# Kernel tuning notes

Measured on AMD Instinct MI355X. Metric: run time of the kernel, lower is better.

The kernel has to match this reference:

```python
import jax, jax.numpy as jnp
import numpy as np
from jax import lax

H = W = 128          # feature map size (gen_line_map uses 128x128)
C = 128              # dim_loi
NPTS0 = 32           # n_pts0 samples per line
NPTS1 = 8            # after MaxPool1d(4, stride=4)
TOPK = 50            # n_dyn_junc
SCALE = 5.0          # proposal_lines distance scale


def proposal_lines(md_maps, dis_maps, scale=SCALE):
    h, w = md_maps.shape[1], md_maps.shape[2]
    y0, x0 = jnp.meshgrid(jnp.arange(h, dtype=jnp.float32),
                          jnp.arange(w, dtype=jnp.float32), indexing='ij')
    md_ = (md_maps[0] - 0.5) * np.pi * 2
    st_ = md_maps[1] * np.pi / 2
    ed_ = -md_maps[2] * np.pi / 2
    cs_md, ss_md = jnp.cos(md_), jnp.sin(md_)
    cs_st = jnp.clip(jnp.cos(st_), 0.001, None)
    ss_st = jnp.clip(jnp.sin(st_), 0.001, None)
    cs_ed = jnp.clip(jnp.cos(ed_), 0.001, None)
    ss_ed = jnp.clip(jnp.sin(ed_), None, -0.001)
    y_st = ss_st / cs_st
    y_ed = ss_ed / cs_ed
    d = dis_maps[0] * scale
    x_st = (cs_md - ss_md * y_st) * d
    y_s = (ss_md + cs_md * y_st) * d
    x_ed = (cs_md - ss_md * y_ed) * d
    y_e = (ss_md + cs_md * y_ed) * d
    x_st_f = jnp.clip(x_st + x0, 0.0, w - 1)
    y_st_f = jnp.clip(y_s + y0, 0.0, h - 1)
    x_ed_f = jnp.clip(x_ed + x0, 0.0, w - 1)
    y_ed_f = jnp.clip(y_e + y0, 0.0, h - 1)
    return jnp.stack((x_st_f, y_st_f, x_ed_f, y_ed_f), axis=-1).reshape(-1, 4)


def pooling(feats, lines):
    # feats: [C, H, W]; lines: [N, 4]
    h, w = feats.shape[1], feats.shape[2]
    tspan = jnp.linspace(0.0, 1.0, NPTS0)[None, None, :]           # [1,1,32]
    U, V = lines[:, :2], lines[:, 2:]
    sp = U[:, :, None] * tspan + V[:, :, None] * (1 - tspan) - 0.5  # [N,2,32]
    sp = sp.transpose(0, 2, 1).reshape(-1, 2)                       # [N*32, 2]
    px, py = sp[:, 0], sp[:, 1]
    px0 = jnp.clip(jnp.floor(px), 0.0, w - 1)
    py0 = jnp.clip(jnp.floor(py), 0.0, h - 1)
    px1 = jnp.clip(px0 + 1, 0.0, w - 1)
    py1 = jnp.clip(py0 + 1, 0.0, h - 1)
    px0l, py0l = px0.astype(jnp.int32), py0.astype(jnp.int32)
    px1l, py1l = px1.astype(jnp.int32), py1.astype(jnp.int32)
    # bilinear gather-weight, fused in a single expression: [C, N*32]
    xp = (feats[:, py0l, px0l] * (py1 - py) * (px1 - px)
          + feats[:, py1l, px0l] * (py - py0) * (px1 - px)
          + feats[:, py0l, px1l] * (py1 - py) * (px - px0)
          + feats[:, py1l, px1l] * (py - py0) * (px - px0))
    xp = xp.reshape(C, -1, NPTS0).transpose(1, 0, 2)                # [N, C, 32]
    xp = xp.reshape(xp.shape[0], C, NPTS1, NPTS0 // NPTS1).max(-1)  # MaxPool1d(4,4)
    return xp.reshape(-1, NPTS1 * C)                                # [N, 1024]


def nms(a):
    # F.max_pool2d(a, 3, stride=1, padding=1) then keep local maxima
    ap = lax.reduce_window(a, -jnp.inf, lax.max, (1, 3, 3), (1, 1, 1), 'SAME')
    return a * (a == ap).astype(a.dtype)


def get_junctions(jloc_nms, joff, topk=TOPK):
    h, w = jloc_nms.shape[1], jloc_nms.shape[2]
    scores, index = lax.top_k(jloc_nms.reshape(-1), topk)
    jf = joff.reshape(2, -1)
    y = (index // w).astype(jnp.float32) + jf[1][index] + 0.5
    x = (index % w).astype(jnp.float32) + jf[0][index] + 0.5
    juncs = jnp.stack((x, y), axis=1)                               # [topk, 2]
    return juncs, scores, index


def setup_inputs() -> dict:
    key = jax.random.key(0)
    ks = jax.random.split(key, 12)
    return {
        'md': jax.random.uniform(ks[0], (3, H, W), dtype=jnp.float32),
        'dis': jax.random.uniform(ks[1], (1, H, W), dtype=jnp.float32),
        'res': jax.random.uniform(ks[2], (1, H, W), dtype=jnp.float32),
        'jloc': jax.random.uniform(ks[3], (1, H, W), dtype=jnp.float32),
        'joff': jax.random.uniform(ks[4], (2, H, W), dtype=jnp.float32) - 0.5,
        'feats': jax.random.normal(ks[5], (C, H, W), dtype=jnp.float32),
        'W1': jax.random.normal(ks[6], (1024, C * NPTS1), dtype=jnp.float32) * 0.02,
        'b1': jax.random.normal(ks[7], (1024,), dtype=jnp.float32) * 0.02,
        'W2': jax.random.normal(ks[8], (1024, 1024), dtype=jnp.float32) * 0.02,
        'b2': jax.random.normal(ks[9], (1024,), dtype=jnp.float32) * 0.02,
        'W3': jax.random.normal(ks[10], (1, 1024), dtype=jnp.float32) * 0.02,
        'b3': jax.random.normal(ks[11], (1,), dtype=jnp.float32) * 0.02,
    }


def reference(md, dis, res, jloc, joff, feats, W1, b1, W2, b2, W3, b3):
    # line proposals at 3 residual scales (use_residual=True)
    lines = jnp.concatenate([
        proposal_lines(md, dis + s * res) for s in (-1.0, 0.0, 1.0)
    ], axis=0)                                                      # [3*H*W, 4]
    # LOI bilinear pooling + scoring MLP (self.fc)
    x = pooling(feats, lines)                                       # [N, 1024]
    x = jax.nn.relu(x @ W1.T + b1)
    x = jax.nn.relu(x @ W2.T + b2)
    logits = x @ W3.T + b3                                          # [N, 1]
    # junction decode: NMS + topk + offset gather
    juncs, jscores, _ = get_junctions(nms(jloc), joff, TOPK)
    return logits, juncs, jscores
```

## Files before the change

kernel.cpp:

```cpp
#include <hip/hip_runtime.h>
#include <hip/hip_bf16.h>
#include <math.h>

#define HH 128
#define WW 128
#define HW 16384
#define NL 49152
#define CC 128
#define NPTS0 32
#define NPTS1 8
#define PI_F 3.14159265358979323846f

typedef __attribute__((ext_vector_type(8))) short short8;
typedef __attribute__((ext_vector_type(4))) float f32x4;

__device__ __forceinline__ ushort f2bf(float f) {
    unsigned u = __builtin_bit_cast(unsigned, f);
    unsigned rounding = 0x7FFFu + ((u >> 16) & 1u);
    return (ushort)((u + rounding) >> 16);
}

__device__ __forceinline__ void gload_lds16(const void* gsrc, void* ldst) {
    __builtin_amdgcn_global_load_lds(
        (const __attribute__((address_space(1))) unsigned int*)gsrc,
        (__attribute__((address_space(3))) unsigned int*)ldst,
        16, 0, 0);
}

__device__ __forceinline__ void unpk8(uint4 d, float* f) {
    f[0] = __builtin_bit_cast(float, d.x << 16);
    f[1] = __builtin_bit_cast(float, d.x & 0xFFFF0000u);
    f[2] = __builtin_bit_cast(float, d.y << 16);
    f[3] = __builtin_bit_cast(float, d.y & 0xFFFF0000u);
    f[4] = __builtin_bit_cast(float, d.z << 16);
    f[5] = __builtin_bit_cast(float, d.z & 0xFFFF0000u);
    f[6] = __builtin_bit_cast(float, d.w << 16);
    f[7] = __builtin_bit_cast(float, d.w & 0xFFFF0000u);
}

__global__ __launch_bounds__(256) void k_lines(
    const float* __restrict__ md, const float* __restrict__ dis,
    const float* __restrict__ res, float* __restrict__ lines)
{
    int g = blockIdx.x * 256 + threadIdx.x;
    if (g >= NL) return;
    int s = g / HW;
    int pix = g - s * HW;
    float sf = (float)(s - 1);
    int y = pix >> 7, x = pix & 127;

    float md0 = md[pix], md1 = md[HW + pix], md2 = md[2 * HW + pix];
    float d = (dis[pix] + sf * res[pix]) * 5.0f;

    float md_ = (md0 - 0.5f) * (2.0f * PI_F);
    float st_ = md1 * (0.5f * PI_F);
    float ed_ = -md2 * (0.5f * PI_F);
    float cs_md = cosf(md_), ss_md = sinf(md_);
    float cs_st = fmaxf(cosf(st_), 0.001f);
    float ss_st = fmaxf(sinf(st_), 0.001f);
    float cs_ed = fmaxf(cosf(ed_), 0.001f);
    float ss_ed = fminf(sinf(ed_), -0.001f);
    float y_st = ss_st / cs_st;
    float y_ed = ss_ed / cs_ed;
    float x_st = (cs_md - ss_md * y_st) * d;
    float y_s  = (ss_md + cs_md * y_st) * d;
    float x_ed = (cs_md - ss_md * y_ed) * d;
    float y_e  = (ss_md + cs_md * y_ed) * d;

    float4 o;
    o.x = fminf(fmaxf(x_st + (float)x, 0.0f), 127.0f);
    o.y = fminf(fmaxf(y_s  + (float)y, 0.0f), 127.0f);
    o.z = fminf(fmaxf(x_ed + (float)x, 0.0f), 127.0f);
    o.w = fminf(fmaxf(y_e  + (float)y, 0.0f), 127.0f);
    ((float4*)lines)[g] = o;
}

__global__ void k_transpose(const float* __restrict__ in, ushort* __restrict__ out)
{
    __shared__ float tile[32][33];
    int cb = blockIdx.x;
    int pb = blockIdx.y;
    int tx = threadIdx.x, ty = threadIdx.y;
#pragma unroll
    for (int j = 0; j < 32; j += 8)
        tile[ty + j][tx] = in[(size_t)(cb * 32 + ty + j) * HW + pb * 32 + tx];
    __syncthreads();
#pragma unroll
    for (int j = 0; j < 32; j += 8)
        out[(size_t)(pb * 32 + ty + j) * CC + cb * 32 + tx] = f2bf(tile[tx][ty + j]);
}

__global__ void k_cvt(const float* __restrict__ a, const float* __restrict__ b,
                      ushort* __restrict__ oa, ushort* __restrict__ ob, int n)
{
    int i = blockIdx.x * 256 + threadIdx.x;
    if (i < n) { oa[i] = f2bf(a[i]); ob[i] = f2bf(b[i]); }
}

__global__ __launch_bounds__(128, 2) void k_pool(
    const ushort* __restrict__ ft, const float* __restrict__ lines,
    ushort* __restrict__ X)
{
    __shared__ __align__(16) unsigned smeta[2048];
    const int t = threadIdx.x;
    const int l_loc = t >> 4, c8 = t & 15;
    const int gl0 = blockIdx.x * 8;

#pragma unroll
    for (int e = 0; e < 2; ++e) {
        int s = t + e * 128;
        int ml = s >> 5, sp = s & 31;
        float4 L = ((const float4*)lines)[gl0 + ml];
        float tf = (float)sp * (1.0f / 31.0f);
        float omt = 1.0f - tf;
        float px = L.x * tf + L.z * omt - 0.5f;
        float py = L.y * tf + L.w * omt - 0.5f;
        float px0 = fminf(fmaxf(floorf(px), 0.0f), 127.0f);
        float py0 = fminf(fmaxf(floorf(py), 0.0f), 127.0f);
        float px1 = fminf(px0 + 1.0f, 127.0f);
        float py1 = fminf(py0 + 1.0f, 127.0f);
        int ix0 = (int)px0, iy0 = (int)py0, ix1 = (int)px1, iy1 = (int)py1;
        float4 wv;
        wv.x = (py1 - py) * (px1 - px);
        wv.y = (py  - py0) * (px1 - px);
        wv.z = (py1 - py) * (px  - px0);
        wv.w = (py  - py0) * (px  - px0);
        int o00 = (iy0 * WW + ix0) * (CC * 2);
        int dx  = (ix1 - ix0) * (CC * 2);
        int dy  = (iy1 - iy0) * (WW * CC * 2);
        int4 ov;
        ov.x = o00;
        ov.y = o00 + dy;
        ov.z = o00 + dx;
        ov.w = o00 + dy + dx;
        *(float4*)&smeta[s * 8]     = wv;
        *(int4*)  &smeta[s * 8 + 4] = ov;
    }
    __syncthreads();

    const unsigned coff = (unsigned)(c8 * 16);
    const char* fbase = (const char*)ft;
    float m[8][8];
#pragma unroll
    for (int ch = 0; ch < 8; ++ch)
#pragma unroll
        for (int g = 0; g < 8; ++g) m[ch][g] = -INFINITY;

#pragma unroll
    for (int g = 0; g < 8; ++g) {
#pragma unroll
        for (int j = 0; j < 4; ++j) {
            const unsigned* mp = &smeta[(l_loc * 32 + g * 4 + j) * 8];
            float4 wv = *(const float4*)mp;
            int4  ov = *(const int4*)(mp + 4);
            uint4 d00 = *(const uint4*)(fbase + ((unsigned)ov.x + coff));
            uint4 d10 = *(const uint4*)(fbase + ((unsigned)ov.y + coff));
            uint4 d01 = *(const uint4*)(fbase + ((unsigned)ov.z + coff));
            uint4 d11 = *(const uint4*)(fbase + ((unsigned)ov.w + coff));
            float f00[8], f10[8], f01[8], f11[8];
            unpk8(d00, f00); unpk8(d10, f10); unpk8(d01, f01); unpk8(d11, f11);
#pragma unroll
            for (int ch = 0; ch < 8; ++ch) {
                float v = f00[ch] * wv.x + f10[ch] * wv.y
                        + f01[ch] * wv.z + f11[ch] * wv.w;
                m[ch][g] = fmaxf(m[ch][g], v);
            }
        }
    }

    ushort* Xp = X + (size_t)(gl0 + l_loc) * 1024 + c8 * 64;
#pragma unroll
    for (int ch = 0; ch < 8; ++ch) {
        short8 pk;
#pragma unroll
        for (int g = 0; g < 8; ++g) pk[g] = (short)f2bf(m[ch][g]);
        *(short8*)(Xp + ch * 8) = pk;
    }
}

#define NIT 8
template<int EPI>
__global__ __launch_bounds__(512, 1) void k_gemm2(
    const ushort* __restrict__ A, const ushort* __restrict__ B,
    const float* __restrict__ bias, ushort* __restrict__ Y,
    const float* __restrict__ w3, float* __restrict__ logits,
    int M, int N, int K)
{
    __shared__ __align__(16) ushort lds[65536];
    const int tid = threadIdx.x;
    const int w = tid >> 6, l = tid & 63;
    const int lr = l & 15, kq = l >> 4;
    const int wm = w >> 2, wn = w & 3;

    const int nwg = gridDim.x;
    const int cpx = nwg >> 3;
    const int swzb = (blockIdx.x & 7) * cpx + (blockIdx.x >> 3);
    const int nbn = N >> 8;
    const int m_blk = swzb / nbn;
    const int n_blk = swzb % nbn;
    const int m0 = m_blk << 8, n0 = n_blk << 8;

    const ushort* pA = A + (size_t)m0 * K;
    const ushort* pB = B + (size_t)n0 * K;

    const int rS = tid >> 3;
    const int gS = (tid & 7) ^ (rS & 7);

#define STG(gp, rowoff, kt, regbase) { \
    gload_lds16((gp) + (size_t)((rowoff) + rS) * K + (kt) * 64 + gS * 8, \
                &lds[(regbase) + tid * 8]); \
    gload_lds16((gp) + (size_t)((rowoff) + 64 + rS) * K + (kt) * 64 + gS * 8, \
                &lds[(regbase) + 4096 + tid * 8]); }

#define FBAR { __builtin_amdgcn_sched_barrier(0); __builtin_amdgcn_s_barrier(); \
               __builtin_amdgcn_sched_barrier(0); }

    const int swz0 = ((kq) ^ (lr & 7)) * 8;
    const int swz1 = ((4 + kq) ^ (lr & 7)) * 8;
    int aoff[8], boff[4];
#pragma unroll
    for (int m = 0; m < 8; ++m) aoff[m] = (wm * 128 + m * 16 + lr) * 64;
#pragma unroll
    for (int n = 0; n < 4; ++n) boff[n] = 16384 + (wn * 64 + n * 16 + lr) * 64;

    f32x4 acc[8][4] = {};
    short8 bq0, bq1, bq2, bq3;

#define MF16(MLO, A0, A1, A2, A3) \
    acc[MLO+0][0] = __builtin_amdgcn_mfma_f32_16x16x32_bf16(bq0, A0, acc[MLO+0][0], 0, 0, 0); \
    acc[MLO+0][1] = __builtin_amdgcn_mfma_f32_16x16x32_bf16(bq1, A0, acc[MLO+0][1], 0, 0, 0); \
    acc[MLO+0][2] = __builtin_amdgcn_mfma_f32_16x16x32_bf16(bq2, A0, acc[MLO+0][2], 0, 0, 0); \
    acc[MLO+0][3] = __builtin_amdgcn_mfma_f32_16x16x32_bf16(bq3, A0, acc[MLO+0][3], 0, 0, 0); \
    acc[MLO+1][0] = __builtin_amdgcn_mfma_f32_16x16x32_bf16(bq0, A1, acc[MLO+1][0], 0, 0, 0); \
    acc[MLO+1][1] = __builtin_amdgcn_mfma_f32_16x16x32_bf16(bq1, A1, acc[MLO+1][1], 0, 0, 0); \
    acc[MLO+1][2] = __builtin_amdgcn_mfma_f32_16x16x32_bf16(bq2, A1, acc[MLO+1][2], 0, 0, 0); \
    acc[MLO+1][3] = __builtin_amdgcn_mfma_f32_16x16x32_bf16(bq3, A1, acc[MLO+1][3], 0, 0, 0); \
    acc[MLO+2][0] = __builtin_amdgcn_mfma_f32_16x16x32_bf16(bq0, A2, acc[MLO+2][0], 0, 0, 0); \
    acc[MLO+2][1] = __builtin_amdgcn_mfma_f32_16x16x32_bf16(bq1, A2, acc[MLO+2][1], 0, 0, 0); \
    acc[MLO+2][2] = __builtin_amdgcn_mfma_f32_16x16x32_bf16(bq2, A2, acc[MLO+2][2], 0, 0, 0); \
    acc[MLO+2][3] = __builtin_amdgcn_mfma_f32_16x16x32_bf16(bq3, A2, acc[MLO+2][3], 0, 0, 0); \
    acc[MLO+3][0] = __builtin_amdgcn_mfma_f32_16x16x32_bf16(bq0, A3, acc[MLO+3][0], 0, 0, 0); \
    acc[MLO+3][1] = __builtin_amdgcn_mfma_f32_16x16x32_bf16(bq1, A3, acc[MLO+3][1], 0, 0, 0); \
    acc[MLO+3][2] = __builtin_amdgcn_mfma_f32_16x16x32_bf16(bq2, A3, acc[MLO+3][2], 0, 0, 0); \
    acc[MLO+3][3] = __builtin_amdgcn_mfma_f32_16x16x32_bf16(bq3, A3, acc[MLO+3][3], 0, 0, 0);

    STG(pA, 0,   0, 0);
    STG(pA, 128, 0, 8192);
    STG(pB, 0,   0, 16384);
    STG(pB, 128, 0, 24576);
    STG(pB, 0,   1, 49152);
    asm volatile("s_waitcnt vmcnt(2)" ::: "memory");
    FBAR;

    for (int i = 0; i < NIT; ++i) {
        const int t1 = 2 * i + 1, t2 = 2 * i + 2, t3 = 2 * i + 3;
        const bool pf = (i < NIT - 1);

        bq0 = *(const short8*)&lds[boff[0] + swz0];
        bq1 = *(const short8*)&lds[boff[1] + swz0];
        bq2 = *(const short8*)&lds[boff[2] + swz0];
        bq3 = *(const short8*)&lds[boff[3] + swz0];
        {
            short8 a0 = *(const short8*)&lds[aoff[0] + swz0];
            short8 a1 = *(const short8*)&lds[aoff[1] + swz0];
            short8 a2 = *(const short8*)&lds[aoff[2] + swz0];
            short8 a3 = *(const short8*)&lds[aoff[3] + swz0];
            STG(pB, 128, t1, 57344);
            FBAR;
            __builtin_amdgcn_s_setprio(1); MF16(0, a0, a1, a2, a3) __builtin_amdgcn_s_setprio(0);
            FBAR;
        }
        {
            short8 a4 = *(const short8*)&lds[aoff[4] + swz0];
            short8 a5 = *(const short8*)&lds[aoff[5] + swz0];
            short8 a6 = *(const short8*)&lds[aoff[6] + swz0];
            short8 a7 = *(const short8*)&lds[aoff[7] + swz0];
            STG(pA, 0, t1, 32768);
            FBAR;
            __builtin_amdgcn_s_setprio(1); MF16(4, a4, a5, a6, a7) __builtin_amdgcn_s_setprio(0);
            FBAR;
        }
        bq0 = *(const short8*)&lds[boff[0] + swz1];
        bq1 = *(const short8*)&lds[boff[1] + swz1];
        bq2 = *(const short8*)&lds[boff[2] + swz1];
        bq3 = *(const short8*)&lds[boff[3] + swz1];
        {
            short8 a0 = *(const short8*)&lds[aoff[0] + swz1];
            short8 a1 = *(const short8*)&lds[aoff[1] + swz1];
            short8 a2 = *(const short8*)&lds[aoff[2] + swz1];
            short8 a3 = *(const short8*)&lds[aoff[3] + swz1];
            STG(pA, 128, t1, 40960);
            FBAR;
            __builtin_amdgcn_s_setprio(1); MF16(0, a0, a1, a2, a3) __builtin_amdgcn_s_setprio(0);
            FBAR;
        }
        {
            short8 a4 = *(const short8*)&lds[aoff[4] + swz1];
            short8 a5 = *(const short8*)&lds[aoff[5] + swz1];
            short8 a6 = *(const short8*)&lds[aoff[6] + swz1];
            short8 a7 = *(const short8*)&lds[aoff[7] + swz1];
            if (pf) STG(pB, 0, t2, 16384);
            FBAR;
            __builtin_amdgcn_s_setprio(1); MF16(4, a4, a5, a6, a7) __builtin_amdgcn_s_setprio(0);
            if (pf) { asm volatile("s_waitcnt vmcnt(2)" ::: "memory"); }
            else    { asm volatile("s_waitcnt vmcnt(0)" ::: "memory"); }
            FBAR;
        }
        bq0 = *(const short8*)&lds[32768 + boff[0] + swz0];
        bq1 = *(const short8*)&lds[32768 + boff[1] + swz0];
        bq2 = *(const short8*)&lds[32768 + boff[2] + swz0];
        bq3 = *(const short8*)&lds[32768 + boff[3] + swz0];
        {
            short8 a0 = *(const short8*)&lds[32768 + aoff[0] + swz0];
            short8 a1 = *(const short8*)&lds[32768 + aoff[1] + swz0];
            short8 a2 = *(const short8*)&lds[32768 + aoff[2] + swz0];
            short8 a3 = *(const short8*)&lds[32768 + aoff[3] + swz0];
            if (pf) STG(pB, 128, t2, 24576);
            FBAR;
            __builtin_amdgcn_s_setprio(1); MF16(0, a0, a1, a2, a3) __builtin_amdgcn_s_setprio(0);
            FBAR;
        }
        {
            short8 a4 = *(const short8*)&lds[32768 + aoff[4] + swz0];
            short8 a5 = *(const short8*)&lds[32768 + aoff[5] + swz0];
            short8 a6 = *(const short8*)&lds[32768 + aoff[6] + swz0];
            short8 a7 = *(const short8*)&lds[32768 + aoff[7] + swz0];
            if (pf) STG(pA, 0, t2, 0);
            FBAR;
            __builtin_amdgcn_s_setprio(1); MF16(4, a4, a5, a6, a7) __builtin_amdgcn_s_setprio(0);
            FBAR;
        }
        bq0 = *(const short8*)&lds[32768 + boff[0] + swz1];
        bq1 = *(const short8*)&lds[32768 + boff[1] + swz1];
        bq2 = *(const short8*)&lds[32768 + boff[2] + swz1];
        bq3 = *(const short8*)&lds[32768 + boff[3] + swz1];
        {
            short8 a0 = *(const short8*)&lds[32768 + aoff[0] + swz1];
            short8 a1 = *(const short8*)&lds[32768 + aoff[1] + swz1];
            short8 a2 = *(const short8*)&lds[32768 + aoff[2] + swz1];
            short8 a3 = *(const short8*)&lds[32768 + aoff[3] + swz1];
            if (pf) STG(pA, 128, t2, 8192);
            FBAR;
            __builtin_amdgcn_s_setprio(1); MF16(0, a0, a1, a2, a3) __builtin_amdgcn_s_setprio(0);
            FBAR;
        }
        {
            short8 a4 = *(const short8*)&lds[32768 + aoff[4] + swz1];
            short8 a5 = *(const short8*)&lds[32768 + aoff[5] + swz1];
            short8 a6 = *(const short8*)&lds[32768 + aoff[6] + swz1];
            short8 a7 = *(const short8*)&lds[32768 + aoff[7] + swz1];
            if (pf) STG(pB, 0, t3, 49152);
            FBAR;
            __builtin_amdgcn_s_setprio(1); MF16(4, a4, a5, a6, a7) __builtin_amdgcn_s_setprio(0);
            if (pf) { asm volatile("s_waitcnt vmcnt(2)" ::: "memory"); }
            FBAR;
        }
    }
#undef STG
#undef FBAR
#undef MF16

    if (EPI == 0) {
#pragma unroll
        for (int n = 0; n < 4; ++n) {
            int cbase = n0 + wn * 64 + n * 16 + kq * 4;
            float4 bv4 = *(const float4*)&bias[cbase];
#pragma unroll
            for (int m = 0; m < 8; ++m) {
                int row = m0 + wm * 128 + m * 16 + lr;
                ushort4 pk;
                pk.x = f2bf(fmaxf(acc[m][n][0] + bv4.x, 0.0f));
                pk.y = f2bf(fmaxf(acc[m][n][1] + bv4.y, 0.0f));
                pk.z = f2bf(fmaxf(acc[m][n][2] + bv4.z, 0.0f));
                pk.w = f2bf(fmaxf(acc[m][n][3] + bv4.w, 0.0f));
                *(ushort4*)(Y + (size_t)row * N + cbase) = pk;
            }
        }
    } else {
        float4 bv4[4], w34[4];
#pragma unroll
        for (int n = 0; n < 4; ++n) {
            int cbase = n0 + wn * 64 + n * 16 + kq * 4;
            bv4[n] = *(const float4*)&bias[cbase];
            w34[n] = *(const float4*)&w3[cbase];
        }
#pragma unroll
        for (int m = 0; m < 8; ++m) {
            float s = 0.0f;
#pragma unroll
            for (int n = 0; n < 4; ++n) {
                s += fmaxf(acc[m][n][0] + bv4[n].x, 0.0f) * w34[n].x;
                s += fmaxf(acc[m][n][1] + bv4[n].y, 0.0f) * w34[n].y;
                s += fmaxf(acc[m][n][2] + bv4[n].z, 0.0f) * w34[n].z;
                s += fmaxf(acc[m][n][3] + bv4[n].w, 0.0f) * w34[n].w;
            }
            s += __shfl_xor(s, 16, 64);
            s += __shfl_xor(s, 32, 64);
            if (kq == 0)
                atomicAdd(&logits[m0 + wm * 128 + m * 16 + lr], s);
        }
    }
}

__global__ void k_init_logits(float* __restrict__ logits, const float* __restrict__ b3, int n)
{
    int i = blockIdx.x * 256 + threadIdx.x;
    if (i < n) logits[i] = b3[0];
}

__global__ __launch_bounds__(256) void k_nms_topk(
    const float* __restrict__ jloc, unsigned long long* __restrict__ cand)
{
    __shared__ unsigned long long sk[256];
    const int t = threadIdx.x;
    const int idx = blockIdx.x * 256 + t;
    const int y = idx >> 7, x = idx & 127;
    float cv = jloc[idx];
    float m = cv;
    for (int dy = -1; dy <= 1; ++dy) {
        int yy = y + dy;
        if (yy < 0 || yy > 127) continue;
        for (int dx = -1; dx <= 1; ++dx) {
            int xx = x + dx;
            if (xx < 0 || xx > 127) continue;
            m = fmaxf(m, jloc[(yy << 7) + xx]);
        }
    }
    float nv = (cv == m) ? cv : 0.0f;
    unsigned vb = __builtin_bit_cast(unsigned, nv);
    sk[t] = ((unsigned long long)vb << 32) | (unsigned)(0xFFFFFFFFu - idx);
    __syncthreads();
    for (int k = 2; k <= 256; k <<= 1) {
        for (int j = k >> 1; j >= 1; j >>= 1) {
            int ixj = t ^ j;
            if (ixj > t) {
                unsigned long long a = sk[t], b = sk[ixj];
                bool up = ((t & k) == 0);
                if (up ? (a < b) : (a > b)) { sk[t] = b; sk[ixj] = a; }
            }
            __syncthreads();
        }
    }
    if (t < 64) cand[blockIdx.x * 64 + t] = (t < 50) ? sk[t] : 0ull;
}

__global__ __launch_bounds__(1024) void k_topk_final(
    const unsigned long long* __restrict__ cand,
    const float* __restrict__ joff, float* __restrict__ outj)
{
    __shared__ unsigned long long sk[4096];
    const int t = threadIdx.x;
#pragma unroll
    for (int e = 0; e < 4; ++e) sk[t + (e << 10)] = cand[t + (e << 10)];
    __syncthreads();
    for (int k = 2; k <= 4096; k <<= 1) {
        for (int j = k >> 1; j >= 1; j >>= 1) {
#pragma unroll
            for (int e = 0; e < 4; ++e) {
                int i = t + (e << 10);
                int ixj = i ^ j;
                if (ixj > i) {
                    unsigned long long a = sk[i], b = sk[ixj];
                    bool up = ((i & k) == 0);
                    if (up ? (a < b) : (a > b)) { sk[i] = b; sk[ixj] = a; }
                }
            }
            __syncthreads();
        }
    }
    if (t < 50) {
        unsigned long long kk = sk[t];
        unsigned idx = 0xFFFFFFFFu - (unsigned)(kk & 0xFFFFFFFFull);
        float val = __builtin_bit_cast(float, (unsigned)(kk >> 32));
        int y = idx >> 7, x = idx & 127;
        outj[2 * t]     = (float)x + joff[idx]      + 0.5f;
        outj[2 * t + 1] = (float)y + joff[HW + idx] + 0.5f;
        outj[100 + t]   = val;
    }
}

extern "C" void kernel_launch(void* const* d_in, const int* in_sizes, int n_in,
                              void* d_out, int out_size, void* d_ws, size_t ws_size,
                              hipStream_t stream) {
    const float* md   = (const float*)d_in[0];
    const float* dis  = (const float*)d_in[1];
    const float* res  = (const float*)d_in[2];
    const float* jloc = (const float*)d_in[3];
    const float* joff = (const float*)d_in[4];
    const float* feats= (const float*)d_in[5];
    const float* W1   = (const float*)d_in[6];
    const float* b1   = (const float*)d_in[7];
    const float* W2   = (const float*)d_in[8];
    const float* b2   = (const float*)d_in[9];
    const float* W3   = (const float*)d_in[10];
    const float* b3   = (const float*)d_in[11];
    float* out = (float*)d_out;

    char* ws = (char*)d_ws;
    size_t off = 0;
    auto alloc = [&](size_t bytes) {
        void* p = ws + off;
        off = (off + bytes + 255) & ~(size_t)255;
        return p;
    };
    float*  lines = (float*) alloc((size_t)NL * 4 * sizeof(float));
    ushort* ft    = (ushort*)alloc((size_t)HW * CC * 2);
    ushort* W1b   = (ushort*)alloc((size_t)1024 * 1024 * 2);
    ushort* W2b   = (ushort*)alloc((size_t)1024 * 1024 * 2);
    ushort* X     = (ushort*)alloc((size_t)NL * 1024 * 2);
    ushort* Y1    = (ushort*)alloc((size_t)NL * 1024 * 2);
    unsigned long long* cand = (unsigned long long*)alloc(4096 * 8);

    k_lines<<<NL / 256, 256, 0, stream>>>(md, dis, res, lines);
    k_transpose<<<dim3(CC / 32, HW / 32), dim3(32, 8), 0, stream>>>(feats, ft);
    k_cvt<<<(1024 * 1024) / 256, 256, 0, stream>>>(W1, W2, W1b, W2b, 1024 * 1024);
    k_pool<<<NL / 8, 128, 0, stream>>>(ft, lines, X);

    int ngrid = (NL / 256) * (1024 / 256);
    k_gemm2<0><<<ngrid, 512, 0, stream>>>(X, W1b, b1, Y1, nullptr, nullptr, NL, 1024, 1024);
    k_init_logits<<<NL / 256, 256, 0, stream>>>(out, b3, NL);
    k_gemm2<1><<<ngrid, 512, 0, stream>>>(Y1, W2b, b2, nullptr, W3, out, NL, 1024, 1024);

    k_nms_topk<<<64, 256, 0, stream>>>(jloc, cand);
    k_topk_final<<<1, 1024, 0, stream>>>(cand, joff, out + NL);
}
```

Measured before the change: 350.4 us.

## Split GEMM 256x256 tile across 16 waves instead of 8

Runs each 256x256 GEMM tile with 1024 threads (16 waves) rather than 512, so each wave owns a 64x64 sub-tile with half the accumulators. Each thread now issues one global-to-LDS load per stage instead of two, and the vmcnt waits are adjusted to match. The aim is more waves per CU to hide LDS and memory latency. The cost is more barrier participants, more LDS reads per MFMA since each wave reuses its B fragments over fewer A rows, and a register budget capped by the 1024-thread launch bound.

```diff
diff --git a/kernel.cpp b/kernel.cpp
--- a/kernel.cpp
+++ b/kernel.cpp
@@ -180,7 +180,7 @@
 
 #define NIT 8
 template<int EPI>
-__global__ __launch_bounds__(512, 1) void k_gemm2(
+__global__ __launch_bounds__(1024) void k_gemm2(
     const ushort* __restrict__ A, const ushort* __restrict__ B,
     const float* __restrict__ bias, ushort* __restrict__ Y,
     const float* __restrict__ w3, float* __restrict__ logits,
@@ -206,27 +206,25 @@
     const int rS = tid >> 3;
     const int gS = (tid & 7) ^ (rS & 7);
 
-#define STG(gp, rowoff, kt, regbase) { \
+#define STG(gp, rowoff, kt, regbase) \
     gload_lds16((gp) + (size_t)((rowoff) + rS) * K + (kt) * 64 + gS * 8, \
-                &lds[(regbase) + tid * 8]); \
-    gload_lds16((gp) + (size_t)((rowoff) + 64 + rS) * K + (kt) * 64 + gS * 8, \
-                &lds[(regbase) + 4096 + tid * 8]); }
+                &lds[(regbase) + tid * 8]);
 
 #define FBAR { __builtin_amdgcn_sched_barrier(0); __builtin_amdgcn_s_barrier(); \
                __builtin_amdgcn_sched_barrier(0); }
 
     const int swz0 = ((kq) ^ (lr & 7)) * 8;
     const int swz1 = ((4 + kq) ^ (lr & 7)) * 8;
-    int aoff[8], boff[4];
-#pragma unroll
-    for (int m = 0; m < 8; ++m) aoff[m] = (wm * 128 + m * 16 + lr) * 64;
+    int aoff[4], boff[4];
+#pragma unroll
+    for (int m = 0; m < 4; ++m) aoff[m] = (wm * 64 + m * 16 + lr) * 64;
 #pragma unroll
     for (int n = 0; n < 4; ++n) boff[n] = 16384 + (wn * 64 + n * 16 + lr) * 64;
 
-    f32x4 acc[8][4] = {};
+    f32x4 acc[4][4] = {};
     short8 bq0, bq1, bq2, bq3;
 
-#define MF16(MLO, A0, A1, A2, A3) \
+#define MF8(MLO, A0, A1) \
     acc[MLO+0][0] = __builtin_amdgcn_mfma_f32_16x16x32_bf16(bq0, A0, acc[MLO+0][0], 0, 0, 0); \
     acc[MLO+0][1] = __builtin_amdgcn_mfma_f32_16x16x32_bf16(bq1, A0, acc[MLO+0][1], 0, 0, 0); \
     acc[MLO+0][2] = __builtin_amdgcn_mfma_f32_16x16x32_bf16(bq2, A0, acc[MLO+0][2], 0, 0, 0); \
@@ -234,22 +232,14 @@
     acc[MLO+1][0] = __builtin_amdgcn_mfma_f32_16x16x32_bf16(bq0, A1, acc[MLO+1][0], 0, 0, 0); \
     acc[MLO+1][1] = __builtin_amdgcn_mfma_f32_16x16x32_bf16(bq1, A1, acc[MLO+1][1], 0, 0, 0); \
     acc[MLO+1][2] = __builtin_amdgcn_mfma_f32_16x16x32_bf16(bq2, A1, acc[MLO+1][2], 0, 0, 0); \
-    acc[MLO+1][3] = __builtin_amdgcn_mfma_f32_16x16x32_bf16(bq3, A1, acc[MLO+1][3], 0, 0, 0); \
-    acc[MLO+2][0] = __builtin_amdgcn_mfma_f32_16x16x32_bf16(bq0, A2, acc[MLO+2][0], 0, 0, 0); \
-    acc[MLO+2][1] = __builtin_amdgcn_mfma_f32_16x16x32_bf16(bq1, A2, acc[MLO+2][1], 0, 0, 0); \
-    acc[MLO+2][2] = __builtin_amdgcn_mfma_f32_16x16x32_bf16(bq2, A2, acc[MLO+2][2], 0, 0, 0); \
-    acc[MLO+2][3] = __builtin_amdgcn_mfma_f32_16x16x32_bf16(bq3, A2, acc[MLO+2][3], 0, 0, 0); \
-    acc[MLO+3][0] = __builtin_amdgcn_mfma_f32_16x16x32_bf16(bq0, A3, acc[MLO+3][0], 0, 0, 0); \
-    acc[MLO+3][1] = __builtin_amdgcn_mfma_f32_16x16x32_bf16(bq1, A3, acc[MLO+3][1], 0, 0, 0); \
-    acc[MLO+3][2] = __builtin_amdgcn_mfma_f32_16x16x32_bf16(bq2, A3, acc[MLO+3][2], 0, 0, 0); \
-    acc[MLO+3][3] = __builtin_amdgcn_mfma_f32_16x16x32_bf16(bq3, A3, acc[MLO+3][3], 0, 0, 0);
+    acc[MLO+1][3] = __builtin_amdgcn_mfma_f32_16x16x32_bf16(bq3, A1, acc[MLO+1][3], 0, 0, 0);
 
     STG(pA, 0,   0, 0);
     STG(pA, 128, 0, 8192);
     STG(pB, 0,   0, 16384);
     STG(pB, 128, 0, 24576);
     STG(pB, 0,   1, 49152);
-    asm volatile("s_waitcnt vmcnt(2)" ::: "memory");
+    asm volatile("s_waitcnt vmcnt(1)" ::: "memory");
     FBAR;
 
     for (int i = 0; i < NIT; ++i) {
@@ -263,21 +253,17 @@
         {
             short8 a0 = *(const short8*)&lds[aoff[0] + swz0];
             short8 a1 = *(const short8*)&lds[aoff[1] + swz0];
+            STG(pB, 128, t1, 57344);
+            FBAR;
+            __builtin_amdgcn_s_setprio(1); MF8(0, a0, a1) __builtin_amdgcn_s_setprio(0);
+            FBAR;
+        }
+        {
             short8 a2 = *(const short8*)&lds[aoff[2] + swz0];
             short8 a3 = *(const short8*)&lds[aoff[3] + swz0];
-            STG(pB, 128, t1, 57344);
-            FBAR;
-            __builtin_amdgcn_s_setprio(1); MF16(0, a0, a1, a2, a3) __builtin_amdgcn_s_setprio(0);
-            FBAR;
-        }
-        {
-            short8 a4 = *(const short8*)&lds[aoff[4] + swz0];
-            short8 a5 = *(const short8*)&lds[aoff[5] + swz0];
-            short8 a6 = *(const short8*)&lds[aoff[6] + swz0];
-            short8 a7 = *(const short8*)&lds[aoff[7] + swz0];
             STG(pA, 0, t1, 32768);
             FBAR;
-            __builtin_amdgcn_s_setprio(1); MF16(4, a4, a5, a6, a7) __builtin_amdgcn_s_setprio(0);
+            __builtin_amdgcn_s_setprio(1); MF8(2, a2, a3) __builtin_amdgcn_s_setprio(0);
             FBAR;
         }
         bq0 = *(const short8*)&lds[boff[0] + swz1];
@@ -287,22 +273,18 @@
         {
             short8 a0 = *(const short8*)&lds[aoff[0] + swz1];
             short8 a1 = *(const short8*)&lds[aoff[1] + swz1];
+            STG(pA, 128, t1, 40960);
+            FBAR;
+            __builtin_amdgcn_s_setprio(1); MF8(0, a0, a1) __builtin_amdgcn_s_setprio(0);
+            FBAR;
+        }
+        {
             short8 a2 = *(const short8*)&lds[aoff[2] + swz1];
             short8 a3 = *(const short8*)&lds[aoff[3] + swz1];
-            STG(pA, 128, t1, 40960);
-            FBAR;
-            __builtin_amdgcn_s_setprio(1); MF16(0, a0, a1, a2, a3) __builtin_amdgcn_s_setprio(0);
-            FBAR;
-        }
-        {
-            short8 a4 = *(const short8*)&lds[aoff[4] + swz1];
-            short8 a5 = *(const short8*)&lds[aoff[5] + swz1];
-            short8 a6 = *(const short8*)&lds[aoff[6] + swz1];
-            short8 a7 = *(const short8*)&lds[aoff[7] + swz1];
             if (pf) STG(pB, 0, t2, 16384);
             FBAR;
-            __builtin_amdgcn_s_setprio(1); MF16(4, a4, a5, a6, a7) __builtin_amdgcn_s_setprio(0);
-            if (pf) { asm volatile("s_waitcnt vmcnt(2)" ::: "memory"); }
+            __builtin_amdgcn_s_setprio(1); MF8(2, a2, a3) __builtin_amdgcn_s_setprio(0);
+            if (pf) { asm volatile("s_waitcnt vmcnt(1)" ::: "memory"); }
             else    { asm volatile("s_waitcnt vmcnt(0)" ::: "memory"); }
             FBAR;
         }
@@ -313,21 +295,17 @@
         {
             short8 a0 = *(const short8*)&lds[32768 + aoff[0] + swz0];
             short8 a1 = *(const short8*)&lds[32768 + aoff[1] + swz0];
+            if (pf) STG(pB, 128, t2, 24576);
+            FBAR;
+            __builtin_amdgcn_s_setprio(1); MF8(0, a0, a1) __builtin_amdgcn_s_setprio(0);
+            FBAR;
+        }
+        {
             short8 a2 = *(const short8*)&lds[32768 + aoff[2] + swz0];
             short8 a3 = *(const short8*)&lds[32768 + aoff[3] + swz0];
-            if (pf) STG(pB, 128, t2, 24576);
-            FBAR;
-            __builtin_amdgcn_s_setprio(1); MF16(0, a0, a1, a2, a3) __builtin_amdgcn_s_setprio(0);
-            FBAR;
-        }
-        {
-            short8 a4 = *(const short8*)&lds[32768 + aoff[4] + swz0];
-            short8 a5 = *(const short8*)&lds[32768 + aoff[5] + swz0];
-            short8 a6 = *(const short8*)&lds[32768 + aoff[6] + swz0];
-            short8 a7 = *(const short8*)&lds[32768 + aoff[7] + swz0];
             if (pf) STG(pA, 0, t2, 0);
             FBAR;
-            __builtin_amdgcn_s_setprio(1); MF16(4, a4, a5, a6, a7) __builtin_amdgcn_s_setprio(0);
+            __builtin_amdgcn_s_setprio(1); MF8(2, a2, a3) __builtin_amdgcn_s_setprio(0);
             FBAR;
         }
         bq0 = *(const short8*)&lds[32768 + boff[0] + swz1];
@@ -337,28 +315,24 @@
         {
             short8 a0 = *(const short8*)&lds[32768 + aoff[0] + swz1];
             short8 a1 = *(const short8*)&lds[32768 + aoff[1] + swz1];
+            if (pf) STG(pA, 128, t2, 8192);
+            FBAR;
+            __builtin_amdgcn_s_setprio(1); MF8(0, a0, a1) __builtin_amdgcn_s_setprio(0);
+            FBAR;
+        }
+        {
             short8 a2 = *(const short8*)&lds[32768 + aoff[2] + swz1];
             short8 a3 = *(const short8*)&lds[32768 + aoff[3] + swz1];
-            if (pf) STG(pA, 128, t2, 8192);
-            FBAR;
-            __builtin_amdgcn_s_setprio(1); MF16(0, a0, a1, a2, a3) __builtin_amdgcn_s_setprio(0);
-            FBAR;
-        }
-        {
-            short8 a4 = *(const short8*)&lds[32768 + aoff[4] + swz1];
-            short8 a5 = *(const short8*)&lds[32768 + aoff[5] + swz1];
-            short8 a6 = *(const short8*)&lds[32768 + aoff[6] + swz1];
-            short8 a7 = *(const short8*)&lds[32768 + aoff[7] + swz1];
             if (pf) STG(pB, 0, t3, 49152);
             FBAR;
-            __builtin_amdgcn_s_setprio(1); MF16(4, a4, a5, a6, a7) __builtin_amdgcn_s_setprio(0);
-            if (pf) { asm volatile("s_waitcnt vmcnt(2)" ::: "memory"); }
+            __builtin_amdgcn_s_setprio(1); MF8(2, a2, a3) __builtin_amdgcn_s_setprio(0);
+            if (pf) { asm volatile("s_waitcnt vmcnt(1)" ::: "memory"); }
             FBAR;
         }
     }
 #undef STG
 #undef FBAR
-#undef MF16
+#undef MF8
 
     if (EPI == 0) {
 #pragma unroll
@@ -366,8 +340,8 @@
             int cbase = n0 + wn * 64 + n * 16 + kq * 4;
             float4 bv4 = *(const float4*)&bias[cbase];
 #pragma unroll
-            for (int m = 0; m < 8; ++m) {
-                int row = m0 + wm * 128 + m * 16 + lr;
+            for (int m = 0; m < 4; ++m) {
+                int row = m0 + wm * 64 + m * 16 + lr;
                 ushort4 pk;
                 pk.x = f2bf(fmaxf(acc[m][n][0] + bv4.x, 0.0f));
                 pk.y = f2bf(fmaxf(acc[m][n][1] + bv4.y, 0.0f));
@@ -385,7 +359,7 @@
             w34[n] = *(const float4*)&w3[cbase];
         }
 #pragma unroll
-        for (int m = 0; m < 8; ++m) {
+        for (int m = 0; m < 4; ++m) {
             float s = 0.0f;
 #pragma unroll
             for (int n = 0; n < 4; ++n) {
@@ -397,7 +371,7 @@
             s += __shfl_xor(s, 16, 64);
             s += __shfl_xor(s, 32, 64);
             if (kq == 0)
-                atomicAdd(&logits[m0 + wm * 128 + m * 16 + lr], s);
+                atomicAdd(&logits[m0 + wm * 64 + m * 16 + lr], s);
         }
     }
 }
@@ -517,9 +491,9 @@
     k_pool<<<NL / 8, 128, 0, stream>>>(ft, lines, X);
 
     int ngrid = (NL / 256) * (1024 / 256);
-    k_gemm2<0><<<ngrid, 512, 0, stream>>>(X, W1b, b1, Y1, nullptr, nullptr, NL, 1024, 1024);
+    k_gemm2<0><<<ngrid, 1024, 0, stream>>>(X, W1b, b1, Y1, nullptr, nullptr, NL, 1024, 1024);
     k_init_logits<<<NL / 256, 256, 0, stream>>>(out, b3, NL);
-    k_gemm2<1><<<ngrid, 512, 0, stream>>>(Y1, W2b, b2, nullptr, W3, out, NL, 1024, 1024);
+    k_gemm2<1><<<ngrid, 1024, 0, stream>>>(Y1, W2b, b2, nullptr, W3, out, NL, 1024, 1024);
 
     k_nms_topk<<<64, 256, 0, stream>>>(jloc, cand);
     k_topk_final<<<1, 1024, 0, stream>>>(cand, joff, out + NL);
```

New measurement: 384.4 us. +9.7%, slower.

## Make GEMM persistent over three M tiles with continuous cross-tile prefetch

Applied to the files above, without the earlier changes.

Grid goes from 768 to 256 workgroups (one per CU on MI355X). Each workgroup walks three consecutive 256-row M tiles against a fixed 256-column N tile, running 24 K-iterations instead of 8. The global-to-LDS prefetch pipeline runs across tile boundaries. The epilogue (bias, ReLU, store or logit dot-product) and accumulator reset are done in-loop every 8 iterations. This is meant to remove the tail effect of 3 waves and the pipeline prologue/drain per tile, and to keep the B tile hot. The cost is an epilogue stall inside the pipelined loop and M/N/grid sizes that are now hard-coded.

```diff
diff --git a/kernel.cpp b/kernel.cpp
--- a/kernel.cpp
+++ b/kernel.cpp
@@ -178,7 +178,7 @@
     }
 }
 
-#define NIT 8
+#define NIT 24
 template<int EPI>
 __global__ __launch_bounds__(512, 1) void k_gemm2(
     const ushort* __restrict__ A, const ushort* __restrict__ B,
@@ -192,24 +192,27 @@
     const int lr = l & 15, kq = l >> 4;
     const int wm = w >> 2, wn = w & 3;
 
-    const int nwg = gridDim.x;
-    const int cpx = nwg >> 3;
+    const int cpx = 256 >> 3;
     const int swzb = (blockIdx.x & 7) * cpx + (blockIdx.x >> 3);
-    const int nbn = N >> 8;
-    const int m_blk = swzb / nbn;
-    const int n_blk = swzb % nbn;
-    const int m0 = m_blk << 8, n0 = n_blk << 8;
-
-    const ushort* pA = A + (size_t)m0 * K;
+    const int n_blk = swzb & 3;
+    const int m_base = (swzb >> 2) * 3;
+    const int n0 = n_blk << 8;
+
+    const ushort* pA = A + (size_t)(m_base << 8) * K;
     const ushort* pB = B + (size_t)n0 * K;
 
     const int rS = tid >> 3;
     const int gS = (tid & 7) ^ (rS & 7);
 
-#define STG(gp, rowoff, kt, regbase) { \
-    gload_lds16((gp) + (size_t)((rowoff) + rS) * K + (kt) * 64 + gS * 8, \
+#define STG_A(tt, rowoff, regbase) { \
+    gload_lds16(pA + (size_t)(((tt) >> 4) * 256 + (rowoff) + rS) * K + ((tt) & 15) * 64 + gS * 8, \
                 &lds[(regbase) + tid * 8]); \
-    gload_lds16((gp) + (size_t)((rowoff) + 64 + rS) * K + (kt) * 64 + gS * 8, \
+    gload_lds16(pA + (size_t)(((tt) >> 4) * 256 + (rowoff) + 64 + rS) * K + ((tt) & 15) * 64 + gS * 8, \
+                &lds[(regbase) + 4096 + tid * 8]); }
+#define STG_B(tt, rowoff, regbase) { \
+    gload_lds16(pB + (size_t)((rowoff) + rS) * K + ((tt) & 15) * 64 + gS * 8, \
+                &lds[(regbase) + tid * 8]); \
+    gload_lds16(pB + (size_t)((rowoff) + 64 + rS) * K + ((tt) & 15) * 64 + gS * 8, \
                 &lds[(regbase) + 4096 + tid * 8]); }
 
 #define FBAR { __builtin_amdgcn_sched_barrier(0); __builtin_amdgcn_s_barrier(); \
@@ -244,11 +247,11 @@
     acc[MLO+3][2] = __builtin_amdgcn_mfma_f32_16x16x32_bf16(bq2, A3, acc[MLO+3][2], 0, 0, 0); \
     acc[MLO+3][3] = __builtin_amdgcn_mfma_f32_16x16x32_bf16(bq3, A3, acc[MLO+3][3], 0, 0, 0);
 
-    STG(pA, 0,   0, 0);
-    STG(pA, 128, 0, 8192);
-    STG(pB, 0,   0, 16384);
-    STG(pB, 128, 0, 24576);
-    STG(pB, 0,   1, 49152);
+    STG_A(0, 0,   0);
+    STG_A(0, 128, 8192);
+    STG_B(0, 0,   16384);
+    STG_B(0, 128, 24576);
+    STG_B(1, 0,   49152);
     asm volatile("s_waitcnt vmcnt(2)" ::: "memory");
     FBAR;
 
@@ -265,7 +268,7 @@
             short8 a1 = *(const short8*)&lds[aoff[1] + swz0];
             short8 a2 = *(const short8*)&lds[aoff[2] + swz0];
             short8 a3 = *(const short8*)&lds[aoff[3] + swz0];
-            STG(pB, 128, t1, 57344);
+            STG_B(t1, 128, 57344);
             FBAR;
             __builtin_amdgcn_s_setprio(1); MF16(0, a0, a1, a2, a3) __builtin_amdgcn_s_setprio(0);
             FBAR;
@@ -275,7 +278,7 @@
             short8 a5 = *(const short8*)&lds[aoff[5] + swz0];
             short8 a6 = *(const short8*)&lds[aoff[6] + swz0];
             short8 a7 = *(const short8*)&lds[aoff[7] + swz0];
-            STG(pA, 0, t1, 32768);
+            STG_A(t1, 0, 32768);
             FBAR;
             __builtin_amdgcn_s_setprio(1); MF16(4, a4, a5, a6, a7) __builtin_amdgcn_s_setprio(0);
             FBAR;
@@ -289,7 +292,7 @@
             short8 a1 = *(const short8*)&lds[aoff[1] + swz1];
             short8 a2 = *(const short8*)&lds[aoff[2] + swz1];
             short8 a3 = *(const short8*)&lds[aoff[3] + swz1];
-            STG(pA, 128, t1, 40960);
+            STG_A(t1, 128, 40960);
             FBAR;
             __builtin_amdgcn_s_setprio(1); MF16(0, a0, a1, a2, a3) __builtin_amdgcn_s_setprio(0);
             FBAR;
@@ -299,7 +302,7 @@
             short8 a5 = *(const short8*)&lds[aoff[5] + swz1];
             short8 a6 = *(const short8*)&lds[aoff[6] + swz1];
             short8 a7 = *(const short8*)&lds[aoff[7] + swz1];
-            if (pf) STG(pB, 0, t2, 16384);
+            if (pf) STG_B(t2, 0, 16384);
             FBAR;
             __builtin_amdgcn_s_setprio(1); MF16(4, a4, a5, a6, a7) __builtin_amdgcn_s_setprio(0);
             if (pf) { asm volatile("s_waitcnt vmcnt(2)" ::: "memory"); }
@@ -315,7 +318,7 @@
             short8 a1 = *(const short8*)&lds[32768 + aoff[1] + swz0];
             short8 a2 = *(const short8*)&lds[32768 + aoff[2] + swz0];
             short8 a3 = *(const short8*)&lds[32768 + aoff[3] + swz0];
-            if (pf) STG(pB, 128, t2, 24576);
+            if (pf) STG_B(t2, 128, 24576);
             FBAR;
             __builtin_amdgcn_s_setprio(1); MF16(0, a0, a1, a2, a3) __builtin_amdgcn_s_setprio(0);
             FBAR;
@@ -325,7 +328,7 @@
             short8 a5 = *(const short8*)&lds[32768 + aoff[5] + swz0];
             short8 a6 = *(const short8*)&lds[32768 + aoff[6] + swz0];
             short8 a7 = *(const short8*)&lds[32768 + aoff[7] + swz0];
-            if (pf) STG(pA, 0, t2, 0);
+            if (pf) STG_A(t2, 0, 0);
             FBAR;
             __builtin_amdgcn_s_setprio(1); MF16(4, a4, a5, a6, a7) __builtin_amdgcn_s_setprio(0);
             FBAR;
@@ -339,7 +342,7 @@
             short8 a1 = *(const short8*)&lds[32768 + aoff[1] + swz1];
             short8 a2 = *(const short8*)&lds[32768 + aoff[2] + swz1];
             short8 a3 = *(const short8*)&lds[32768 + aoff[3] + swz1];
-            if (pf) STG(pA, 128, t2, 8192);
+            if (pf) STG_A(t2, 128, 8192);
             FBAR;
             __builtin_amdgcn_s_setprio(1); MF16(0, a0, a1, a2, a3) __builtin_amdgcn_s_setprio(0);
             FBAR;
@@ -349,57 +352,67 @@
             short8 a5 = *(const short8*)&lds[32768 + aoff[5] + swz1];
             short8 a6 = *(const short8*)&lds[32768 + aoff[6] + swz1];
             short8 a7 = *(const short8*)&lds[32768 + aoff[7] + swz1];
-            if (pf) STG(pB, 0, t3, 49152);
+            if (pf) STG_B(t3, 0, 49152);
             FBAR;
             __builtin_amdgcn_s_setprio(1); MF16(4, a4, a5, a6, a7) __builtin_amdgcn_s_setprio(0);
             if (pf) { asm volatile("s_waitcnt vmcnt(2)" ::: "memory"); }
             FBAR;
         }
-    }
-#undef STG
+
+        if ((i & 7) == 7) {
+            const int j = i >> 3;
+            const int m0j = (m_base + j) << 8;
+            if (EPI == 0) {
+#pragma unroll
+                for (int n = 0; n < 4; ++n) {
+                    int cbase = n0 + wn * 64 + n * 16 + kq * 4;
+                    float4 bv4 = *(const float4*)&bias[cbase];
+#pragma unroll
+                    for (int m = 0; m < 8; ++m) {
+                        int row = m0j + wm * 128 + m * 16 + lr;
+                        ushort4 pk;
+                        pk.x = f2bf(fmaxf(acc[m][n][0] + bv4.x, 0.0f));
+                        pk.y = f2bf(fmaxf(acc[m][n][1] + bv4.y, 0.0f));
+                        pk.z = f2bf(fmaxf(acc[m][n][2] + bv4.z, 0.0f));
+                        pk.w = f2bf(fmaxf(acc[m][n][3] + bv4.w, 0.0f));
+                        *(ushort4*)(Y + (size_t)row * N + cbase) = pk;
+                    }
+                }
+            } else {
+                float4 bv4[4], w34[4];
+#pragma unroll
+                for (int n = 0; n < 4; ++n) {
+                    int cbase = n0 + wn * 64 + n * 16 + kq * 4;
+                    bv4[n] = *(const float4*)&bias[cbase];
+                    w34[n] = *(const float4*)&w3[cbase];
+                }
+#pragma unroll
+                for (int m = 0; m < 8; ++m) {
+                    float s = 0.0f;
+#pragma unroll
+                    for (int n = 0; n < 4; ++n) {
+                        s += fmaxf(acc[m][n][0] + bv4[n].x, 0.0f) * w34[n].x;
+                        s += fmaxf(acc[m][n][1] + bv4[n].y, 0.0f) * w34[n].y;
+                        s += fmaxf(acc[m][n][2] + bv4[n].z, 0.0f) * w34[n].z;
+                        s += fmaxf(acc[m][n][3] + bv4[n].w, 0.0f) * w34[n].w;
+                    }
+                    s += __shfl_xor(s, 16, 64);
+                    s += __shfl_xor(s, 32, 64);
+                    if (kq == 0)
+                        atomicAdd(&logits[m0j + wm * 128 + m * 16 + lr], s);
+                }
+            }
+#pragma unroll
+            for (int m = 0; m < 8; ++m)
+#pragma unroll
+                for (int n = 0; n < 4; ++n)
+                    acc[m][n] = (f32x4){0.0f, 0.0f, 0.0f, 0.0f};
+        }
+    }
+#undef STG_A
+#undef STG_B
 #undef FBAR
 #undef MF16
-
-    if (EPI == 0) {
-#pragma unroll
-        for (int n = 0; n < 4; ++n) {
-            int cbase = n0 + wn * 64 + n * 16 + kq * 4;
-            float4 bv4 = *(const float4*)&bias[cbase];
-#pragma unroll
-            for (int m = 0; m < 8; ++m) {
-                int row = m0 + wm * 128 + m * 16 + lr;
-                ushort4 pk;
-                pk.x = f2bf(fmaxf(acc[m][n][0] + bv4.x, 0.0f));
-                pk.y = f2bf(fmaxf(acc[m][n][1] + bv4.y, 0.0f));
-                pk.z = f2bf(fmaxf(acc[m][n][2] + bv4.z, 0.0f));
-                pk.w = f2bf(fmaxf(acc[m][n][3] + bv4.w, 0.0f));
-                *(ushort4*)(Y + (size_t)row * N + cbase) = pk;
-            }
-        }
-    } else {
-        float4 bv4[4], w34[4];
-#pragma unroll
-        for (int n = 0; n < 4; ++n) {
-            int cbase = n0 + wn * 64 + n * 16 + kq * 4;
-            bv4[n] = *(const float4*)&bias[cbase];
-            w34[n] = *(const float4*)&w3[cbase];
-        }
-#pragma unroll
-        for (int m = 0; m < 8; ++m) {
-            float s = 0.0f;
-#pragma unroll
-            for (int n = 0; n < 4; ++n) {
-                s += fmaxf(acc[m][n][0] + bv4[n].x, 0.0f) * w34[n].x;
-                s += fmaxf(acc[m][n][1] + bv4[n].y, 0.0f) * w34[n].y;
-                s += fmaxf(acc[m][n][2] + bv4[n].z, 0.0f) * w34[n].z;
-                s += fmaxf(acc[m][n][3] + bv4[n].w, 0.0f) * w34[n].w;
-            }
-            s += __shfl_xor(s, 16, 64);
-            s += __shfl_xor(s, 32, 64);
-            if (kq == 0)
-                atomicAdd(&logits[m0 + wm * 128 + m * 16 + lr], s);
-        }
-    }
 }
 
 __global__ void k_init_logits(float* __restrict__ logits, const float* __restrict__ b3, int n)
@@ -516,10 +529,9 @@
     k_cvt<<<(1024 * 1024) / 256, 256, 0, stream>>>(W1, W2, W1b, W2b, 1024 * 1024);
     k_pool<<<NL / 8, 128, 0, stream>>>(ft, lines, X);
 
-    int ngrid = (NL / 256) * (1024 / 256);
-    k_gemm2<0><<<ngrid, 512, 0, stream>>>(X, W1b, b1, Y1, nullptr, nullptr, NL, 1024, 1024);
+    k_gemm2<0><<<256, 512, 0, stream>>>(X, W1b, b1, Y1, nullptr, nullptr, NL, 1024, 1024);
     k_init_logits<<<NL / 256, 256, 0, stream>>>(out, b3, NL);
-    k_gemm2<1><<<ngrid, 512, 0, stream>>>(Y1, W2b, b2, nullptr, W3, out, NL, 1024, 1024);
+    k_gemm2<1><<<256, 512, 0, stream>>>(Y1, W2b, b2, nullptr, W3, out, NL, 1024, 1024);
 
     k_nms_topk<<<64, 256, 0, stream>>>(jloc, cand);
     k_topk_final<<<1, 1024, 0, stream>>>(cand, joff, out + NL);
```

Result: no change. 350.9 us (+0.1%).
